# Kernel optimization log

Hardware: AMD Instinct MI355X
Metric: run time of the kernel (lower is better)

Reference implementation:

```python
import jax, jax.numpy as jnp
import numpy as np

N_NODES = 100000
N_EDGES = 1600000
IN_DIM = 128
HID = 128
OUT = 128
NUM_GRAPHS = 2048


def setup_inputs() -> dict:
    key = jax.random.key(0)
    ks = jax.random.split(key, 10)
    x = jax.random.normal(ks[0], (N_NODES, IN_DIM), dtype=jnp.float32)
    edge_index = jax.random.randint(ks[1], (2, N_EDGES), 0, N_NODES, dtype=jnp.int32)
    graph_index = jnp.sort(jax.random.randint(ks[2], (N_NODES,), 0, NUM_GRAPHS, dtype=jnp.int32))
    def glorot(k, fi, fo):
        lim = jnp.sqrt(6.0 / (fi + fo)).astype(jnp.float32)
        return jax.random.uniform(k, (fi, fo), jnp.float32, -lim, lim)
    return {
        "x": x,
        "edge_index": edge_index,
        "graph_index": graph_index,
        "num_graphs": NUM_GRAPHS,
        "W1": glorot(ks[3], IN_DIM, HID), "b1": jnp.zeros((HID,), jnp.float32),
        "W2": glorot(ks[4], HID, HID),    "b2": jnp.zeros((HID,), jnp.float32),
        "W3": glorot(ks[5], HID, OUT),    "b3": jnp.zeros((OUT,), jnp.float32),
    }


def _gcn_layer(x, src, dst, norm, W, b, n_nodes):
    # transform first (cheap GEMM), then normalized gather-scatter aggregation
    h = x @ W                              # [N, F]
    msg = h[src] * norm[:, None]           # [E+N, F] gather + scale
    out = jax.ops.segment_sum(msg, dst, num_segments=n_nodes)  # scatter-add
    return out + b


def reference(x, edge_index, graph_index, num_graphs, W1, b1, W2, b2, W3, b3):
    n = x.shape[0]
    # add self-loops (PyG GCNConv default)
    loops = jnp.arange(n, dtype=edge_index.dtype)
    src = jnp.concatenate([edge_index[0], loops])
    dst = jnp.concatenate([edge_index[1], loops])
    # symmetric normalization D^-1/2 (A+I) D^-1/2, degree = in-degree incl. self-loop
    deg = jax.ops.segment_sum(jnp.ones_like(src, dtype=x.dtype), dst, num_segments=n)
    dinv = jax.lax.rsqrt(jnp.maximum(deg, 1.0))
    norm = dinv[src] * dinv[dst]
    # 3 conv layers + ReLU (dropout = identity at inference)
    h = jax.nn.relu(_gcn_layer(x, src, dst, norm, W1, b1, n))
    h = jax.nn.relu(_gcn_layer(h, src, dst, norm, W2, b2, n))
    h = jax.nn.relu(_gcn_layer(h, src, dst, norm, W3, b3, n))
    # global mean / max pooling per graph
    gsum = jax.ops.segment_sum(h, graph_index, num_segments=num_graphs)
    cnt = jax.ops.segment_sum(jnp.ones((n,), h.dtype), graph_index, num_segments=num_graphs)
    gmean = gsum / jnp.maximum(cnt, 1.0)[:, None]
    gmax = jax.ops.segment_max(h, graph_index, num_segments=num_graphs)
    return jnp.concatenate([gmean, gmax], axis=-1)
```

## Files before the change

kernel.cpp:

```cpp
#include <hip/hip_runtime.h>
#include <hip/hip_bf16.h>
#include <stdint.h>

#define N_NODES   100000
#define N_EDGES   1600000
#define FDIM      128
#define NUM_GR    2048
#define CSR_CAP   64

#define NBKT      391
#define BKT_CAP   4864
#define TILE      4096
#define LBIN_CAP  32
#define LBIN_STR  33

typedef __attribute__((ext_vector_type(8))) short short8;
typedef __attribute__((ext_vector_type(4))) float f32x4;

__device__ __forceinline__ uint32_t pk2(float a, float b) {
    __hip_bfloat16 x = __float2bfloat16(a), y = __float2bfloat16(b);
    uint16_t ux = *reinterpret_cast<uint16_t*>(&x);
    uint16_t uy = *reinterpret_cast<uint16_t*>(&y);
    return (uint32_t)ux | ((uint32_t)uy << 16);
}

__device__ __forceinline__ float bflo(uint32_t u) { return __uint_as_float(u << 16); }
__device__ __forceinline__ float bfhi(uint32_t u) { return __uint_as_float(u & 0xFFFF0000u); }


__global__ __launch_bounds__(256) void k_fused1(
        const float* __restrict__ x, const float* __restrict__ W1,
        __hip_bfloat16* __restrict__ C, int n, int gGemm,
        const int* __restrict__ src, const int* __restrict__ dst,
        int* __restrict__ bkt_cnt, int* __restrict__ bkt, int E, int gA,
        const float* __restrict__ W2, const float* __restrict__ W3,
        __hip_bfloat16* __restrict__ wt) {
    __shared__ uint32_t smem[16384];
    const int b = blockIdx.x;
    const int tid = threadIdx.x;

    if (b >= gGemm + gA) {
        int idx = 16384 + (b - gGemm - gA) * 256 + tid;
        int l = idx >> 14, rem = idx & 16383, c = rem >> 7, k = rem & 127;
        const float* W = (l == 1) ? W2 : W3;
        wt[idx] = __float2bfloat16(W[k * FDIM + c]);
        return;
    }

    if (b >= gGemm) {
        int* binCnt  = (int*)smem;
        int* binBase = (int*)smem + NBKT;
        int* bins    = (int*)smem + 2 * NBKT;
        int bb = b - gGemm;

        for (int i = tid; i < NBKT; i += 256) binCnt[i] = 0;
        __syncthreads();

        int e0 = bb * TILE;
        int e1 = min(E, e0 + TILE);
        for (int e = e0 + tid; e < e1; e += 256) {
            int s = src[e];
            int d = dst[e];
            int bi = d >> 8;
            int rec = ((d & 255) << 17) | s;
            int pos = atomicAdd(&binCnt[bi], 1);
            if (pos < LBIN_CAP) {
                bins[bi * LBIN_STR + pos] = rec;
            } else {
                int gp = atomicAdd(&bkt_cnt[bi], 1);
                if (gp < BKT_CAP) bkt[bi * BKT_CAP + gp] = rec;
            }
        }
        __syncthreads();

        for (int i = tid; i < NBKT; i += 256) {
            int c = min(binCnt[i], LBIN_CAP);
            binBase[i] = (c > 0) ? atomicAdd(&bkt_cnt[i], c) : 0;
        }
        __syncthreads();

        for (int i = tid; i < NBKT * LBIN_CAP; i += 256) {
            int bi = i / LBIN_CAP, sl = i - bi * LBIN_CAP;
            if (sl < min(binCnt[bi], LBIN_CAP)) {
                int gp = binBase[bi] + sl;
                if (gp < BKT_CAP) bkt[bi * BKT_CAP + gp] = bins[bi * LBIN_STR + sl];
            }
        }
        return;
    }

    uint32_t* Atl = smem;
    uint32_t* Wtl = smem + 128 * 64;

    const int rowBase = b * 128;

    for (int it = 0; it < 16; ++it) {
        int g = it * 256 + tid;
        int r = g >> 5;
        int seg = g & 31;
        float4 v = make_float4(0.f, 0.f, 0.f, 0.f);
        if (rowBase + r < n) v = *(const float4*)&x[(size_t)(rowBase + r) * FDIM + seg * 4];
        int gg = seg >> 1;
        int word = r * 64 + (((gg ^ (r & 7)) << 2) | ((seg & 1) << 1));
        uint2 pv;
        pv.x = pk2(v.x, v.y);
        pv.y = pk2(v.z, v.w);
        *(uint2*)&Atl[word] = pv;
    }
    for (int it = 0; it < 32; ++it) {
        int idx = it * 256 + tid;
        int kp = idx >> 7;
        int c  = idx & 127;
        float w0 = W1[(size_t)(2 * kp) * FDIM + c];
        float w1 = W1[(size_t)(2 * kp + 1) * FDIM + c];
        int word = c * 64 + ((((kp >> 2) ^ (c & 7)) << 2) | (kp & 3));
        Wtl[word] = pk2(w0, w1);
    }
    __syncthreads();

    const int w = tid >> 6;
    const int lane = tid & 63;
    const int r = lane & 15;
    const int q = lane >> 4;

    f32x4 acc[8][2] = {};

#pragma unroll
    for (int kk = 0; kk < 4; ++kk) {
        int gr = ((kk * 4 + q) ^ (r & 7)) << 2;
        short8 a0 = *(const short8*)&Atl[(w * 32 + r) * 64 + gr];
        short8 a1 = *(const short8*)&Atl[(w * 32 + 16 + r) * 64 + gr];
#pragma unroll
        for (int m = 0; m < 8; ++m) {
            short8 bw = *(const short8*)&Wtl[(m * 16 + r) * 64 + gr];
            acc[m][0] = __builtin_amdgcn_mfma_f32_16x16x32_bf16(bw, a0, acc[m][0], 0, 0, 0);
            acc[m][1] = __builtin_amdgcn_mfma_f32_16x16x32_bf16(bw, a1, acc[m][1], 0, 0, 0);
        }
    }

#pragma unroll
    for (int nt = 0; nt < 2; ++nt) {
        int node = rowBase + w * 32 + nt * 16 + r;
        if (node < n) {
#pragma unroll
            for (int m = 0; m < 8; ++m) {
                f32x4 v = acc[m][nt];
                uint2 pv;
                pv.x = pk2(v[0], v[1]);
                pv.y = pk2(v[2], v[3]);
                *(uint2*)&C[(size_t)node * FDIM + m * 16 + q * 4] = pv;
            }
        }
    }
}


__global__ __launch_bounds__(256) void k_csr(const int* __restrict__ bkt_cnt,
                                             const int* __restrict__ bkt,
                                             int* __restrict__ cnt,
                                             float* __restrict__ dinv,
                                             int* __restrict__ csr, int n) {
    __shared__ int lc[64];
    __shared__ int cur[64];
    int b = blockIdx.x;
    int tid = threadIdx.x;
    int bi = b >> 2;
    int qd = b & 3;

    if (b == 0 && tid == 0) dinv[n] = 0.f;

    if (tid < 64) { lc[tid] = 0; cur[tid] = 0; }
    __syncthreads();

    int len = min(bkt_cnt[bi], BKT_CAP);
    const int* recs = bkt + bi * BKT_CAP;

    for (int i = tid; i < len; i += 256) {
        int dl = (recs[i] >> 17) & 255;
        if ((dl >> 6) == qd) atomicAdd(&lc[dl & 63], 1);
    }
    __syncthreads();

    if (tid < 64) {
        int v = (bi << 8) + (qd << 6) + tid;
        if (v < n) {
            int c = lc[tid];
            cnt[v] = c;
            dinv[v] = rsqrtf((float)(c + 1));
        }
    }

    for (int i = tid; i < len; i += 256) {
        int rec = recs[i];
        int dl = (rec >> 17) & 255;
        if ((dl >> 6) == qd) {
            int pos = atomicAdd(&cur[dl & 63], 1);
            if (pos < CSR_CAP)
                csr[(((size_t)(bi << 8) + dl) << 6) + pos] = rec & 0x1FFFF;
        }
    }
}


__global__ __launch_bounds__(256) void k_gemm(const __hip_bfloat16* __restrict__ Ap,
                                              const __hip_bfloat16* __restrict__ Wt,
                                              const float* __restrict__ dinv,
                                              __hip_bfloat16* __restrict__ C, int n) {
    __shared__ uint32_t lds[2 * 128 * 64];
    uint32_t* Atl = lds;
    uint32_t* Wtl = lds + 128 * 64;

    const int tid = threadIdx.x;
    const int rowBase = blockIdx.x * 128;

    const uint4* A4 = (const uint4*)Ap;
    for (int it = 0; it < 8; ++it) {
        int g = it * 256 + tid;
        int r = g >> 4;
        int seg = g & 15;
        uint4 v = make_uint4(0, 0, 0, 0);
        if (rowBase + r < n) v = A4[((size_t)rowBase + r) * 16 + seg];
        int word = r * 64 + ((seg ^ (r & 7)) << 2);
        *(uint4*)&Atl[word] = v;
    }
    for (int it = 0; it < 8; ++it) {
        int g = it * 256 + tid;
        int r = g >> 4;
        int seg = g & 15;
        uint4 v = *(const uint4*)&Wt[(size_t)r * FDIM + seg * 8];
        int word = r * 64 + ((seg ^ (r & 7)) << 2);
        *(uint4*)&Wtl[word] = v;
    }
    __syncthreads();

    const int w = tid >> 6;
    const int lane = tid & 63;
    const int r = lane & 15;
    const int q = lane >> 4;

    f32x4 acc[8][2] = {};

#pragma unroll
    for (int kk = 0; kk < 4; ++kk) {
        int gr = ((kk * 4 + q) ^ (r & 7)) << 2;
        short8 a0 = *(const short8*)&Atl[(w * 32 + r) * 64 + gr];
        short8 a1 = *(const short8*)&Atl[(w * 32 + 16 + r) * 64 + gr];
#pragma unroll
        for (int m = 0; m < 8; ++m) {
            short8 bw = *(const short8*)&Wtl[(m * 16 + r) * 64 + gr];
            acc[m][0] = __builtin_amdgcn_mfma_f32_16x16x32_bf16(bw, a0, acc[m][0], 0, 0, 0);
            acc[m][1] = __builtin_amdgcn_mfma_f32_16x16x32_bf16(bw, a1, acc[m][1], 0, 0, 0);
        }
    }

#pragma unroll
    for (int nt = 0; nt < 2; ++nt) {
        int node = rowBase + w * 32 + nt * 16 + r;
        if (node < n) {
            float dv = dinv[node];
#pragma unroll
            for (int m = 0; m < 8; ++m) {
                f32x4 v = acc[m][nt];
                uint2 pv;
                pv.x = pk2(v[0] * dv, v[1] * dv);
                pv.y = pk2(v[2] * dv, v[3] * dv);
                *(uint2*)&C[(size_t)node * FDIM + m * 16 + q * 4] = pv;
            }
        }
    }
}


template<int WEIGHTED>
__global__ __launch_bounds__(256) void k_agg(const __hip_bfloat16* __restrict__ T,
                                             const int* __restrict__ cnt,
                                             const int* __restrict__ csr,
                                             const float* __restrict__ dinv,
                                             const float* __restrict__ bias,
                                             uint32_t* __restrict__ Hb,
                                             int n) {
    int wid = (blockIdx.x * 256 + threadIdx.x) >> 6;
    int lane = threadIdx.x & 63;
    if (wid >= n) return;
    int v = wid;
    int g   = lane >> 4;
    int s16 = lane & 15;

    const uint4* Tu4 = (const uint4*)T;

    int cv  = min(cnt[v], CSR_CAP);
    int sraw = csr[((size_t)v << 6) + lane];
    int sidx = (lane < cv) ? sraw : ((lane == cv) ? v : n);
    cv += 1;

    float a0 = 0.f, a1 = 0.f, a2 = 0.f, a3 = 0.f;
    float a4 = 0.f, a5 = 0.f, a6 = 0.f, a7 = 0.f;

    int mr = (cv + 15) & ~15;
    for (int j = 0; j < mr; j += 16) {
        uint4 gg[4];
        float wv[4];
#pragma unroll
        for (int t = 0; t < 4; ++t) {
            int it = __shfl(sidx, j + 4 * t + g, 64);
            if constexpr (WEIGHTED) wv[t] = dinv[it];
            gg[t] = Tu4[(size_t)it * 16 + s16];
        }
#pragma unroll
        for (int t = 0; t < 4; ++t) {
            if constexpr (WEIGHTED) {
                a0 = fmaf(wv[t], bflo(gg[t].x), a0); a1 = fmaf(wv[t], bfhi(gg[t].x), a1);
                a2 = fmaf(wv[t], bflo(gg[t].y), a2); a3 = fmaf(wv[t], bfhi(gg[t].y), a3);
                a4 = fmaf(wv[t], bflo(gg[t].z), a4); a5 = fmaf(wv[t], bfhi(gg[t].z), a5);
                a6 = fmaf(wv[t], bflo(gg[t].w), a6); a7 = fmaf(wv[t], bfhi(gg[t].w), a7);
            } else {
                a0 += bflo(gg[t].x); a1 += bfhi(gg[t].x);
                a2 += bflo(gg[t].y); a3 += bfhi(gg[t].y);
                a4 += bflo(gg[t].z); a5 += bfhi(gg[t].z);
                a6 += bflo(gg[t].w); a7 += bfhi(gg[t].w);
            }
        }
    }

    a0 += __shfl_xor(a0, 16, 64); a0 += __shfl_xor(a0, 32, 64);
    a1 += __shfl_xor(a1, 16, 64); a1 += __shfl_xor(a1, 32, 64);
    a2 += __shfl_xor(a2, 16, 64); a2 += __shfl_xor(a2, 32, 64);
    a3 += __shfl_xor(a3, 16, 64); a3 += __shfl_xor(a3, 32, 64);
    a4 += __shfl_xor(a4, 16, 64); a4 += __shfl_xor(a4, 32, 64);
    a5 += __shfl_xor(a5, 16, 64); a5 += __shfl_xor(a5, 32, 64);
    a6 += __shfl_xor(a6, 16, 64); a6 += __shfl_xor(a6, 32, 64);
    a7 += __shfl_xor(a7, 16, 64); a7 += __shfl_xor(a7, 32, 64);

    if (g == 0) {
        float dv = dinv[v];
        float4 bb0 = *(const float4*)&bias[s16 * 8];
        float4 bb1 = *(const float4*)&bias[s16 * 8 + 4];
        float r0 = fmaxf(fmaf(dv, a0, bb0.x), 0.f);
        float r1 = fmaxf(fmaf(dv, a1, bb0.y), 0.f);
        float r2 = fmaxf(fmaf(dv, a2, bb0.z), 0.f);
        float r3 = fmaxf(fmaf(dv, a3, bb0.w), 0.f);
        float r4 = fmaxf(fmaf(dv, a4, bb1.x), 0.f);
        float r5 = fmaxf(fmaf(dv, a5, bb1.y), 0.f);
        float r6 = fmaxf(fmaf(dv, a6, bb1.z), 0.f);
        float r7 = fmaxf(fmaf(dv, a7, bb1.w), 0.f);
        uint4 pv;
        pv.x = pk2(r0, r1);
        pv.y = pk2(r2, r3);
        pv.z = pk2(r4, r5);
        pv.w = pk2(r6, r7);
        *(uint4*)&Hb[(size_t)v * 64 + s16 * 4] = pv;
    }
}


__device__ __forceinline__ int lower_bound_dev(const int* a, int n, int key) {
    int lo = 0, hi = n;
    while (lo < hi) {
        int m = (lo + hi) >> 1;
        if (a[m] < key) lo = m + 1; else hi = m;
    }
    return lo;
}

__global__ __launch_bounds__(256) void k_pool2(const uint32_t* __restrict__ Hb,
                                               const int* __restrict__ gidx,
                                               float* __restrict__ out, int n) {
    __shared__ float ls0[256], ls1[256], lm0[256], lm1[256];
    int g = blockIdx.x;
    int w = threadIdx.x >> 6;
    int lane = threadIdx.x & 63;

    int lo = lower_bound_dev(gidx, n, g);
    int hi = lower_bound_dev(gidx, n, g + 1);

    float s0 = 0.f, s1 = 0.f, m0 = 0.f, m1 = 0.f;
    for (int v = lo + w; v < hi; v += 4) {
        uint32_t u = Hb[(size_t)v * 64 + lane];
        float x0 = bflo(u), x1 = bfhi(u);
        s0 += x0; s1 += x1;
        m0 = fmaxf(m0, x0); m1 = fmaxf(m1, x1);
    }
    ls0[threadIdx.x] = s0; ls1[threadIdx.x] = s1;
    lm0[threadIdx.x] = m0; lm1[threadIdx.x] = m1;
    __syncthreads();

    if (w == 0) {
#pragma unroll
        for (int ww = 1; ww < 4; ++ww) {
            s0 += ls0[ww * 64 + lane]; s1 += ls1[ww * 64 + lane];
            m0 = fmaxf(m0, lm0[ww * 64 + lane]);
            m1 = fmaxf(m1, lm1[ww * 64 + lane]);
        }
        float inv = 1.f / (float)max(hi - lo, 1);
        float* og = out + (size_t)g * 2 * FDIM;
        og[lane * 2]     = s0 * inv;
        og[lane * 2 + 1] = s1 * inv;
        og[FDIM + lane * 2]     = m0;
        og[FDIM + lane * 2 + 1] = m1;
    }
}


extern "C" void kernel_launch(void* const* d_in, const int* in_sizes, int n_in,
                              void* d_out, int out_size, void* d_ws, size_t ws_size,
                              hipStream_t stream) {
    const float* x    = (const float*)d_in[0];
    const int*   ei   = (const int*)d_in[1];
    const int*   gidx = (const int*)d_in[2];
    const float* W1 = (const float*)d_in[4];
    const float* b1 = (const float*)d_in[5];
    const float* W2 = (const float*)d_in[6];
    const float* b2 = (const float*)d_in[7];
    const float* W3 = (const float*)d_in[8];
    const float* b3 = (const float*)d_in[9];
    float* out = (float*)d_out;

    const int N = N_NODES, E = N_EDGES;
    const int* src = ei;
    const int* dst = ei + E;

    char* ws = (char*)d_ws;
    size_t o = 0;
    auto alloc = [&](size_t bytes) { size_t r = o; o += (bytes + 255) & ~(size_t)255; return r; };
    size_t o_bktcnt = alloc((size_t)NBKT * 4);
    size_t o_bkt    = alloc((size_t)NBKT * BKT_CAP * 4);
    size_t o_cnt    = alloc((size_t)N * 4);
    size_t o_dinv   = alloc((size_t)(N + 1) * 4);
    size_t o_csr    = alloc((size_t)NBKT * 256 * CSR_CAP * 4);
    size_t o_wt     = alloc((size_t)3 * FDIM * FDIM * 2);
    size_t o_t      = alloc((size_t)(N + 1) * FDIM * 2);
    size_t o_h      = alloc((size_t)N * FDIM * 2);

    int*   bkt_cnt = (int*)(ws + o_bktcnt);
    int*   bkt     = (int*)(ws + o_bkt);
    int*   cnt     = (int*)(ws + o_cnt);
    float* dinv    = (float*)(ws + o_dinv);
    int*   csr     = (int*)(ws + o_csr);
    __hip_bfloat16* wtbuf = (__hip_bfloat16*)(ws + o_wt);
    __hip_bfloat16* tbuf  = (__hip_bfloat16*)(ws + o_t);
    __hip_bfloat16* hb16  = (__hip_bfloat16*)(ws + o_h);

    hipMemsetAsync(bkt_cnt, 0, (size_t)NBKT * 4, stream);
    hipMemsetAsync(tbuf + (size_t)N * FDIM, 0, FDIM * 2, stream);

    const int gA    = (E + TILE - 1) / TILE;
    const int gGemm = (N + 127) / 128;

    k_fused1<<<gGemm + gA + 128, 256, 0, stream>>>(x, W1, tbuf, N, gGemm,
                                                   src, dst, bkt_cnt, bkt, E, gA,
                                                   W2, W3, wtbuf);
    k_csr<<<NBKT * 4, 256, 0, stream>>>(bkt_cnt, bkt, cnt, dinv, csr, N);

    const int gAgg = (N + 3) / 4;

    k_agg<1><<<gAgg, 256, 0, stream>>>(tbuf, cnt, csr, dinv, b1, (uint32_t*)hb16, N);
    k_gemm<<<gGemm, 256, 0, stream>>>(hb16, wtbuf + FDIM * FDIM, dinv, tbuf, N);
    k_agg<0><<<gAgg, 256, 0, stream>>>(tbuf, cnt, csr, dinv, b2, (uint32_t*)hb16, N);
    k_gemm<<<gGemm, 256, 0, stream>>>(hb16, wtbuf + 2 * FDIM * FDIM, dinv, tbuf, N);
    k_agg<0><<<gAgg, 256, 0, stream>>>(tbuf, cnt, csr, dinv, b3, (uint32_t*)hb16, N);

    k_pool2<<<NUM_GR, 256, 0, stream>>>((const uint32_t*)hb16, gidx, out, N);
}
```

Before: 403.5 us.

## Fuse pooling into last aggregation and load GEMM A operands directly from global

The final aggregation kernel now does graph mean/max pooling itself, using LDS and float atomics into a zeroed output with per-graph reciprocal counts precomputed by extra blocks in the first fused kernel. This removes the separate pool kernel and the bf16 write and read of the last hidden layer. Both GEMM kernels drop the A-tile staging through LDS and read A fragments straight from global memory, halving shared memory so more blocks fit per CU (launch bounds set to 4). The local bin capacity in the bucketing pass is also halved to fit the smaller shared buffer. The trade-off is many atomics on the output, possible nondeterministic sums, and uncoalesced global reads in the GEMMs.

```diff
diff --git a/kernel.cpp b/kernel.cpp
--- a/kernel.cpp
+++ b/kernel.cpp
@@ -11,8 +11,8 @@
 #define NBKT      391
 #define BKT_CAP   4864
 #define TILE      4096
-#define LBIN_CAP  32
-#define LBIN_STR  33
+#define LBIN_CAP  16
+#define LBIN_STR  17
 
 typedef __attribute__((ext_vector_type(8))) short short8;
 typedef __attribute__((ext_vector_type(4))) float f32x4;
@@ -27,17 +27,46 @@
 __device__ __forceinline__ float bflo(uint32_t u) { return __uint_as_float(u << 16); }
 __device__ __forceinline__ float bfhi(uint32_t u) { return __uint_as_float(u & 0xFFFF0000u); }
 
-
-__global__ __launch_bounds__(256) void k_fused1(
+__device__ __forceinline__ short8 pack8(float4 u0, float4 u1) {
+    union { uint32_t u[4]; short8 s; } cv;
+    cv.u[0] = pk2(u0.x, u0.y);
+    cv.u[1] = pk2(u0.z, u0.w);
+    cv.u[2] = pk2(u1.x, u1.y);
+    cv.u[3] = pk2(u1.z, u1.w);
+    return cv.s;
+}
+
+__device__ __forceinline__ int lower_bound_dev(const int* a, int n, int key) {
+    int lo = 0, hi = n;
+    while (lo < hi) {
+        int m = (lo + hi) >> 1;
+        if (a[m] < key) lo = m + 1; else hi = m;
+    }
+    return lo;
+}
+
+
+__global__ __launch_bounds__(256, 4) void k_fused1(
         const float* __restrict__ x, const float* __restrict__ W1,
         __hip_bfloat16* __restrict__ C, int n, int gGemm,
         const int* __restrict__ src, const int* __restrict__ dst,
         int* __restrict__ bkt_cnt, int* __restrict__ bkt, int E, int gA,
         const float* __restrict__ W2, const float* __restrict__ W3,
-        __hip_bfloat16* __restrict__ wt) {
-    __shared__ uint32_t smem[16384];
+        __hip_bfloat16* __restrict__ wt,
+        const int* __restrict__ gidx, float* __restrict__ gscale) {
+    __shared__ uint32_t smem[8192];
     const int b = blockIdx.x;
     const int tid = threadIdx.x;
+
+    if (b >= gGemm + gA + 128) {
+        int g = (b - (gGemm + gA + 128)) * 256 + tid;
+        if (g < NUM_GR) {
+            int lo = lower_bound_dev(gidx, n, g);
+            int hi = lower_bound_dev(gidx, n, g + 1);
+            gscale[g] = 1.f / (float)max(hi - lo, 1);
+        }
+        return;
+    }
 
     if (b >= gGemm + gA) {
         int idx = 16384 + (b - gGemm - gA) * 256 + tid;
@@ -89,24 +118,10 @@
         return;
     }
 
-    uint32_t* Atl = smem;
-    uint32_t* Wtl = smem + 128 * 64;
+    uint32_t* Wtl = smem;
 
     const int rowBase = b * 128;
 
-    for (int it = 0; it < 16; ++it) {
-        int g = it * 256 + tid;
-        int r = g >> 5;
-        int seg = g & 31;
-        float4 v = make_float4(0.f, 0.f, 0.f, 0.f);
-        if (rowBase + r < n) v = *(const float4*)&x[(size_t)(rowBase + r) * FDIM + seg * 4];
-        int gg = seg >> 1;
-        int word = r * 64 + (((gg ^ (r & 7)) << 2) | ((seg & 1) << 1));
-        uint2 pv;
-        pv.x = pk2(v.x, v.y);
-        pv.y = pk2(v.z, v.w);
-        *(uint2*)&Atl[word] = pv;
-    }
     for (int it = 0; it < 32; ++it) {
         int idx = it * 256 + tid;
         int kp = idx >> 7;
@@ -123,13 +138,19 @@
     const int r = lane & 15;
     const int q = lane >> 4;
 
+    const int r0c = min(rowBase + w * 32 + r, n - 1);
+    const int r1c = min(rowBase + w * 32 + 16 + r, n - 1);
+
     f32x4 acc[8][2] = {};
 
 #pragma unroll
     for (int kk = 0; kk < 4; ++kk) {
+        int co = (kk * 4 + q) * 8;
+        const float4* p0 = (const float4*)&x[(size_t)r0c * FDIM + co];
+        const float4* p1 = (const float4*)&x[(size_t)r1c * FDIM + co];
+        short8 a0 = pack8(p0[0], p0[1]);
+        short8 a1 = pack8(p1[0], p1[1]);
         int gr = ((kk * 4 + q) ^ (r & 7)) << 2;
-        short8 a0 = *(const short8*)&Atl[(w * 32 + r) * 64 + gr];
-        short8 a1 = *(const short8*)&Atl[(w * 32 + 16 + r) * 64 + gr];
 #pragma unroll
         for (int m = 0; m < 8; ++m) {
             short8 bw = *(const short8*)&Wtl[(m * 16 + r) * 64 + gr];
@@ -202,27 +223,15 @@
 }
 
 
-__global__ __launch_bounds__(256) void k_gemm(const __hip_bfloat16* __restrict__ Ap,
-                                              const __hip_bfloat16* __restrict__ Wt,
-                                              const float* __restrict__ dinv,
-                                              __hip_bfloat16* __restrict__ C, int n) {
-    __shared__ uint32_t lds[2 * 128 * 64];
-    uint32_t* Atl = lds;
-    uint32_t* Wtl = lds + 128 * 64;
+__global__ __launch_bounds__(256, 4) void k_gemm(const __hip_bfloat16* __restrict__ Ap,
+                                                 const __hip_bfloat16* __restrict__ Wt,
+                                                 const float* __restrict__ dinv,
+                                                 __hip_bfloat16* __restrict__ C, int n) {
+    __shared__ uint32_t Wtl[128 * 64];
 
     const int tid = threadIdx.x;
     const int rowBase = blockIdx.x * 128;
 
-    const uint4* A4 = (const uint4*)Ap;
-    for (int it = 0; it < 8; ++it) {
-        int g = it * 256 + tid;
-        int r = g >> 4;
-        int seg = g & 15;
-        uint4 v = make_uint4(0, 0, 0, 0);
-        if (rowBase + r < n) v = A4[((size_t)rowBase + r) * 16 + seg];
-        int word = r * 64 + ((seg ^ (r & 7)) << 2);
-        *(uint4*)&Atl[word] = v;
-    }
     for (int it = 0; it < 8; ++it) {
         int g = it * 256 + tid;
         int r = g >> 4;
@@ -238,13 +247,17 @@
     const int r = lane & 15;
     const int q = lane >> 4;
 
+    const uint4* A4 = (const uint4*)Ap;
+    const int r0c = min(rowBase + w * 32 + r, n - 1);
+    const int r1c = min(rowBase + w * 32 + 16 + r, n - 1);
+
     f32x4 acc[8][2] = {};
 
 #pragma unroll
     for (int kk = 0; kk < 4; ++kk) {
+        short8 a0 = *(const short8*)&A4[(size_t)r0c * 16 + kk * 4 + q];
+        short8 a1 = *(const short8*)&A4[(size_t)r1c * 16 + kk * 4 + q];
         int gr = ((kk * 4 + q) ^ (r & 7)) << 2;
-        short8 a0 = *(const short8*)&Atl[(w * 32 + r) * 64 + gr];
-        short8 a1 = *(const short8*)&Atl[(w * 32 + 16 + r) * 64 + gr];
 #pragma unroll
         for (int m = 0; m < 8; ++m) {
             short8 bw = *(const short8*)&Wtl[(m * 16 + r) * 64 + gr];
@@ -271,13 +284,16 @@
 }
 
 
-template<int WEIGHTED>
+template<int WEIGHTED, int POOL>
 __global__ __launch_bounds__(256) void k_agg(const __hip_bfloat16* __restrict__ T,
                                              const int* __restrict__ cnt,
                                              const int* __restrict__ csr,
                                              const float* __restrict__ dinv,
                                              const float* __restrict__ bias,
                                              uint32_t* __restrict__ Hb,
+                                             const int* __restrict__ gidx,
+                                             const float* __restrict__ gscale,
+                                             float* __restrict__ out,
                                              int n) {
     int wid = (blockIdx.x * 256 + threadIdx.x) >> 6;
     int lane = threadIdx.x & 63;
@@ -331,72 +347,67 @@
     a6 += __shfl_xor(a6, 16, 64); a6 += __shfl_xor(a6, 32, 64);
     a7 += __shfl_xor(a7, 16, 64); a7 += __shfl_xor(a7, 32, 64);
 
-    if (g == 0) {
-        float dv = dinv[v];
-        float4 bb0 = *(const float4*)&bias[s16 * 8];
-        float4 bb1 = *(const float4*)&bias[s16 * 8 + 4];
-        float r0 = fmaxf(fmaf(dv, a0, bb0.x), 0.f);
-        float r1 = fmaxf(fmaf(dv, a1, bb0.y), 0.f);
-        float r2 = fmaxf(fmaf(dv, a2, bb0.z), 0.f);
-        float r3 = fmaxf(fmaf(dv, a3, bb0.w), 0.f);
-        float r4 = fmaxf(fmaf(dv, a4, bb1.x), 0.f);
-        float r5 = fmaxf(fmaf(dv, a5, bb1.y), 0.f);
-        float r6 = fmaxf(fmaf(dv, a6, bb1.z), 0.f);
-        float r7 = fmaxf(fmaf(dv, a7, bb1.w), 0.f);
-        uint4 pv;
-        pv.x = pk2(r0, r1);
-        pv.y = pk2(r2, r3);
-        pv.z = pk2(r4, r5);
-        pv.w = pk2(r6, r7);
-        *(uint4*)&Hb[(size_t)v * 64 + s16 * 4] = pv;
-    }
-}
-
-
-__device__ __forceinline__ int lower_bound_dev(const int* a, int n, int key) {
-    int lo = 0, hi = n;
-    while (lo < hi) {
-        int m = (lo + hi) >> 1;
-        if (a[m] < key) lo = m + 1; else hi = m;
-    }
-    return lo;
-}
-
-__global__ __launch_bounds__(256) void k_pool2(const uint32_t* __restrict__ Hb,
-                                               const int* __restrict__ gidx,
-                                               float* __restrict__ out, int n) {
-    __shared__ float ls0[256], ls1[256], lm0[256], lm1[256];
-    int g = blockIdx.x;
-    int w = threadIdx.x >> 6;
-    int lane = threadIdx.x & 63;
-
-    int lo = lower_bound_dev(gidx, n, g);
-    int hi = lower_bound_dev(gidx, n, g + 1);
-
-    float s0 = 0.f, s1 = 0.f, m0 = 0.f, m1 = 0.f;
-    for (int v = lo + w; v < hi; v += 4) {
-        uint32_t u = Hb[(size_t)v * 64 + lane];
-        float x0 = bflo(u), x1 = bfhi(u);
-        s0 += x0; s1 += x1;
-        m0 = fmaxf(m0, x0); m1 = fmaxf(m1, x1);
-    }
-    ls0[threadIdx.x] = s0; ls1[threadIdx.x] = s1;
-    lm0[threadIdx.x] = m0; lm1[threadIdx.x] = m1;
-    __syncthreads();
-
-    if (w == 0) {
-#pragma unroll
-        for (int ww = 1; ww < 4; ++ww) {
-            s0 += ls0[ww * 64 + lane]; s1 += ls1[ww * 64 + lane];
-            m0 = fmaxf(m0, lm0[ww * 64 + lane]);
-            m1 = fmaxf(m1, lm1[ww * 64 + lane]);
-        }
-        float inv = 1.f / (float)max(hi - lo, 1);
-        float* og = out + (size_t)g * 2 * FDIM;
-        og[lane * 2]     = s0 * inv;
-        og[lane * 2 + 1] = s1 * inv;
-        og[FDIM + lane * 2]     = m0;
-        og[FDIM + lane * 2 + 1] = m1;
+    if constexpr (!POOL) {
+        if (g == 0) {
+            float dv = dinv[v];
+            float4 bb0 = *(const float4*)&bias[s16 * 8];
+            float4 bb1 = *(const float4*)&bias[s16 * 8 + 4];
+            float r0 = fmaxf(fmaf(dv, a0, bb0.x), 0.f);
+            float r1 = fmaxf(fmaf(dv, a1, bb0.y), 0.f);
+            float r2 = fmaxf(fmaf(dv, a2, bb0.z), 0.f);
+            float r3 = fmaxf(fmaf(dv, a3, bb0.w), 0.f);
+            float r4 = fmaxf(fmaf(dv, a4, bb1.x), 0.f);
+            float r5 = fmaxf(fmaf(dv, a5, bb1.y), 0.f);
+            float r6 = fmaxf(fmaf(dv, a6, bb1.z), 0.f);
+            float r7 = fmaxf(fmaf(dv, a7, bb1.w), 0.f);
+            uint4 pv;
+            pv.x = pk2(r0, r1);
+            pv.y = pk2(r2, r3);
+            pv.z = pk2(r4, r5);
+            pv.w = pk2(r6, r7);
+            *(uint4*)&Hb[(size_t)v * 64 + s16 * 4] = pv;
+        }
+    } else {
+        __shared__ float lds_h[4 * 128];
+        __shared__ int   lds_g[4];
+        int wave = threadIdx.x >> 6;
+        if (g == 0) {
+            float dv = dinv[v];
+            float4 bb0 = *(const float4*)&bias[s16 * 8];
+            float4 bb1 = *(const float4*)&bias[s16 * 8 + 4];
+            float* hh = &lds_h[wave * 128 + s16 * 8];
+            hh[0] = fmaxf(fmaf(dv, a0, bb0.x), 0.f);
+            hh[1] = fmaxf(fmaf(dv, a1, bb0.y), 0.f);
+            hh[2] = fmaxf(fmaf(dv, a2, bb0.z), 0.f);
+            hh[3] = fmaxf(fmaf(dv, a3, bb0.w), 0.f);
+            hh[4] = fmaxf(fmaf(dv, a4, bb1.x), 0.f);
+            hh[5] = fmaxf(fmaf(dv, a5, bb1.y), 0.f);
+            hh[6] = fmaxf(fmaf(dv, a6, bb1.z), 0.f);
+            hh[7] = fmaxf(fmaf(dv, a7, bb1.w), 0.f);
+            if (s16 == 0) lds_g[wave] = gidx[v];
+        }
+        __syncthreads();
+        if (threadIdx.x < 128) {
+            int f = threadIdx.x;
+            int cg = lds_g[0];
+            float s = 0.f, m = 0.f;
+#pragma unroll
+            for (int ww = 0; ww < 4; ++ww) {
+                int gw = lds_g[ww];
+                float hv = lds_h[ww * 128 + f];
+                if (gw != cg) {
+                    atomicAdd(&out[(size_t)cg * 256 + f], s * gscale[cg]);
+                    atomicMax((unsigned int*)&out[(size_t)cg * 256 + 128 + f],
+                              __float_as_uint(m));
+                    s = 0.f; m = 0.f; cg = gw;
+                }
+                s += hv;
+                m = fmaxf(m, hv);
+            }
+            atomicAdd(&out[(size_t)cg * 256 + f], s * gscale[cg]);
+            atomicMax((unsigned int*)&out[(size_t)cg * 256 + 128 + f],
+                      __float_as_uint(m));
+        }
     }
 }
 
@@ -430,6 +441,7 @@
     size_t o_wt     = alloc((size_t)3 * FDIM * FDIM * 2);
     size_t o_t      = alloc((size_t)(N + 1) * FDIM * 2);
     size_t o_h      = alloc((size_t)N * FDIM * 2);
+    size_t o_gs     = alloc((size_t)NUM_GR * 4);
 
     int*   bkt_cnt = (int*)(ws + o_bktcnt);
     int*   bkt     = (int*)(ws + o_bkt);
@@ -439,25 +451,28 @@
     __hip_bfloat16* wtbuf = (__hip_bfloat16*)(ws + o_wt);
     __hip_bfloat16* tbuf  = (__hip_bfloat16*)(ws + o_t);
     __hip_bfloat16* hb16  = (__hip_bfloat16*)(ws + o_h);
+    float* gscale = (float*)(ws + o_gs);
 
     hipMemsetAsync(bkt_cnt, 0, (size_t)NBKT * 4, stream);
     hipMemsetAsync(tbuf + (size_t)N * FDIM, 0, FDIM * 2, stream);
+    hipMemsetAsync(out, 0, (size_t)NUM_GR * 2 * FDIM * 4, stream);
 
     const int gA    = (E + TILE - 1) / TILE;
     const int gGemm = (N + 127) / 128;
 
-    k_fused1<<<gGemm + gA + 128, 256, 0, stream>>>(x, W1, tbuf, N, gGemm,
-                                                   src, dst, bkt_cnt, bkt, E, gA,
-                                                   W2, W3, wtbuf);
+    k_fused1<<<gGemm + gA + 128 + 8, 256, 0, stream>>>(x, W1, tbuf, N, gGemm,
+                                                       src, dst, bkt_cnt, bkt, E, gA,
+                                                       W2, W3, wtbuf, gidx, gscale);
     k_csr<<<NBKT * 4, 256, 0, stream>>>(bkt_cnt, bkt, cnt, dinv, csr, N);
 
     const int gAgg = (N + 3) / 4;
 
-    k_agg<1><<<gAgg, 256, 0, stream>>>(tbuf, cnt, csr, dinv, b1, (uint32_t*)hb16, N);
+    k_agg<1, 0><<<gAgg, 256, 0, stream>>>(tbuf, cnt, csr, dinv, b1, (uint32_t*)hb16,
+                                          nullptr, nullptr, nullptr, N);
     k_gemm<<<gGemm, 256, 0, stream>>>(hb16, wtbuf + FDIM * FDIM, dinv, tbuf, N);
-    k_agg<0><<<gAgg, 256, 0, stream>>>(tbuf, cnt, csr, dinv, b2, (uint32_t*)hb16, N);
+    k_agg<0, 0><<<gAgg, 256, 0, stream>>>(tbuf, cnt, csr, dinv, b2, (uint32_t*)hb16,
+                                          nullptr, nullptr, nullptr, N);
     k_gemm<<<gGemm, 256, 0, stream>>>(hb16, wtbuf + 2 * FDIM * FDIM, dinv, tbuf, N);
-    k_agg<0><<<gAgg, 256, 0, stream>>>(tbuf, cnt, csr, dinv, b3, (uint32_t*)hb16, N);
-
-    k_pool2<<<NUM_GR, 256, 0, stream>>>((const uint32_t*)hb16, gidx, out, N);
-}
+    k_agg<0, 1><<<gAgg, 256, 0, stream>>>(tbuf, cnt, csr, dinv, b3, nullptr,
+                                          gidx, gscale, out, N);
+}
```

After: 381.1 us. 1.06x faster.
